# Performance work log

Hardware: AMD Instinct MI355X
Metric: run time of the kernel (lower is better)

The kernel has to match this reference:

```python
import jax, jax.numpy as jnp
import numpy as np

H, DH, RK, RD = 16, 128, 512, 64  # num_heads, head_dim, kv_lora_rank, rope_dim


def apply_rope(x, cos, sin):
    # x: [..., L, ..., rope_dim]; cos/sin: [L, rope_dim//2]
    cos = cos[None, :, None, :]
    sin = sin[None, :, None, :]
    x1, x2 = x[..., 0::2], x[..., 1::2]
    out_real = x1 * cos - x2 * sin
    out_imag = x1 * sin + x2 * cos
    return jnp.stack([out_real, out_imag], axis=-1).reshape(x.shape)


def setup_inputs() -> dict:
    key = jax.random.key(0)
    ks = jax.random.split(key, 7)
    B, L, E, MAXLEN = 2, 2048, 2048, 4096
    x = jax.random.normal(ks[0], (B, L, E), dtype=jnp.float32)
    cos_table = jax.random.uniform(ks[1], (MAXLEN, RD // 2), dtype=jnp.float32)
    sin_table = jax.random.uniform(ks[2], (MAXLEN, RD // 2), dtype=jnp.float32)
    wq = jax.random.normal(ks[3], (E, H * (DH + RD)), dtype=jnp.float32) / np.sqrt(E)
    wkv_down = jax.random.normal(ks[4], (E, RK + RD), dtype=jnp.float32) / np.sqrt(E)
    w_up = jax.random.normal(ks[5], (RK, H * (2 * DH + RD)), dtype=jnp.float32) / np.sqrt(RK)
    w_out = jax.random.normal(ks[6], (H * (DH + RD), E), dtype=jnp.float32) / np.sqrt(H * (DH + RD))
    return {"x": x, "cos_table": cos_table, "sin_table": sin_table,
            "wq": wq, "wkv_down": wkv_down, "w_up": w_up, "w_out": w_out}


def reference(x, cos_table, sin_table, wq, wkv_down, w_up, w_out):
    # Prefill path (use_cache=False): idx = 0, kv comes from current tokens only.
    B, L, E = x.shape
    cos = cos_table[:L]
    sin = sin_table[:L]

    # Queries: per-head content part + rope part
    q_all = (x @ wq).reshape(B, L, H, DH + RD)
    q_head, q_rope = q_all[..., :DH], q_all[..., DH:]
    q_rope = apply_rope(q_rope, cos, sin)
    q = jnp.concatenate([q_head, q_rope], axis=-1)  # [B,L,H,DH+RD]

    # Compressed KV latent + shared rope key
    kv_lat = x @ wkv_down                            # [B,L,RK+RD]
    c_kv = kv_lat[..., :RK]
    k_rope = kv_lat[..., RK:]
    k_rope = apply_rope(k_rope[:, :, None, :], cos, sin)[:, :, 0, :]  # [B,L,RD]

    # Up-project latent to per-head K/V
    up = (c_kv @ w_up).reshape(B, L, H, 2 * DH + RD)
    k_head = up[..., :DH]
    v_head = up[..., DH:2 * DH]
    v_rope = up[..., 2 * DH:]
    k_rope_b = jnp.broadcast_to(k_rope[:, :, None, :], (B, L, H, RD))
    k = jnp.concatenate([k_head, k_rope_b], axis=-1)  # [B,L,H,DH+RD]
    v = jnp.concatenate([v_head, v_rope], axis=-1)    # [B,L,H,DH+RD]

    # Causal attention (query_indices = arange(L), key_indices = arange(L))
    scale = 1.0 / jnp.sqrt(jnp.float32(DH + RD))
    scores = jnp.einsum('blhd,bshd->bhls', q, k) * scale
    idxs = jnp.arange(L)
    bias = jnp.where(idxs[:, None] >= idxs[None, :], 0.0, -1000000000.0)
    attn = jax.nn.softmax(scores + bias[None, None, :, :], axis=-1)
    out = jnp.einsum('bhls,bshd->blhd', attn, v)  # [B,L,H,DH+RD]
    return out.reshape(B, L, -1) @ w_out
```

## Files before the change

### kernel.cpp

```cpp
#include <hip/hip_runtime.h>
#include <stdint.h>

#define H_ 16
#define DH_ 128
#define RK_ 512
#define RD_ 64
#define B_ 2
#define L_ 2048
#define E_ 2048
#define DQ_ 192
#define NQ_ (H_*DQ_)
#define NKV_ 576
#define QKVP_ 3840
#define NUP_ (H_*(2*DH_+RD_))
#define M_ (B_*L_)

typedef unsigned short u16;
typedef __bf16 bf16x8 __attribute__((ext_vector_type(8)));
typedef float floatx4 __attribute__((ext_vector_type(4)));

__device__ __forceinline__ u16 f2bf(float f) {
    union { float f; uint32_t u; } v; v.f = f;
    uint32_t u = v.u;
    u = (u + 0x7fffu + ((u >> 16) & 1u)) >> 16;
    return (u16)u;
}
__device__ __forceinline__ float bf2f(u16 b) {
    union { uint32_t u; float f; } v; v.u = ((uint32_t)b) << 16; return v.f;
}
__device__ __forceinline__ uint32_t cvtpk(float lo, float hi) {
    uint32_t r;
    asm("v_cvt_pk_bf16_f32 %0, %1, %2" : "=v"(r) : "v"(lo), "v"(hi));
    return r;
}

__device__ __forceinline__ void gld_lds16(const void* g, void* l) {
    __builtin_amdgcn_global_load_lds((__attribute__((address_space(1))) void*)(g),
                                     (__attribute__((address_space(3))) void*)(l),
                                     16, 0, 0);
}

__global__ void convert_bf16(const float* __restrict__ in, u16* __restrict__ out, int n4) {
    int i = blockIdx.x * blockDim.x + threadIdx.x;
    if (i >= n4) return;
    float4 v = ((const float4*)in)[i];
    uint2 o;
    o.x = cvtpk(v.x, v.y);
    o.y = cvtpk(v.z, v.w);
    ((uint2*)out)[i] = o;
}

__global__ void transpose_all(const float* __restrict__ wq, const float* __restrict__ wkv,
                              const float* __restrict__ wup, const float* __restrict__ wout,
                              u16* __restrict__ wqkvT, u16* __restrict__ wupT,
                              u16* __restrict__ woutT) {
    __shared__ float tile[32][33];
    int bid = blockIdx.x;
    const float* W; u16* Wt; int K, N, bx, by;
    if (bid < 6144)        { W = wq;   Wt = wqkvT;                      K = 2048; N = 3072; bx = bid % 96;  by = bid / 96; }
    else if (bid < 7680)   { int b = bid - 6144; W = wkv;  Wt = wqkvT + (size_t)3072 * 2048; K = 2048; N = 576;  bx = b % 24;  by = b / 24; }
    else if (bid < 10240)  { int b = bid - 7680; W = wup;  Wt = wupT;   K = 512;  N = 5120; bx = b % 160; by = b / 160; }
    else                   { int b = bid - 10240; W = wout; Wt = woutT; K = 3072; N = 2048; bx = b % 64;  by = b / 64; }
    int n0 = bx * 32, k0 = by * 32;
    int tx = threadIdx.x, ty = threadIdx.y;
    for (int i = 0; i < 4; i++) {
        int k = k0 + ty + i * 8, n = n0 + tx;
        tile[ty + i * 8][tx] = (n < N) ? W[(size_t)k * N + n] : 0.f;
    }
    __syncthreads();
    for (int i = 0; i < 4; i++) {
        int n = n0 + ty + i * 8, k = k0 + tx;
        Wt[(size_t)n * K + k] = f2bf(tile[tx][ty + i * 8]);
    }
}

template<bool BF16OUT>
__global__ __launch_bounds__(512, 4) void gemm256(const u16* __restrict__ A,
                                                  const u16* __restrict__ Bt,
                                                  void* __restrict__ Cv,
                                                  int M, int N, int K, int lda) {
    __shared__ __align__(16) u16 As[3][256 * 32];
    __shared__ __align__(16) u16 Bs[3][128 * 32];
    const int tid = threadIdx.x;
    const int wave = tid >> 6, lane = tid & 63;
    const int quad = lane >> 4, l16 = lane & 15;
    const int wm = (wave >> 1) * 64, wn = (wave & 1) * 64;

    int nwg = gridDim.x * gridDim.y;
    int flat = blockIdx.y * gridDim.x + blockIdx.x;
    int q = nwg >> 3, r = nwg & 7;
    int xcd = flat & 7, pos = flat >> 3;
    int wg = (xcd < r) ? xcd * (q + 1) + pos : r * (q + 1) + (xcd - r) * q + pos;
    const int m0 = (wg & 15) * 256;
    const int n0 = (wg >> 4) * 128;

    const u16* Ab = A + (size_t)m0 * lda;
    const u16* Bb = Bt + (size_t)n0 * K;

    const int qsw = (quad ^ ((l16 >> 1) & 3)) * 8;

    floatx4 zero4 = {0.f, 0.f, 0.f, 0.f};
    floatx4 acc[4][4];
#pragma unroll
    for (int i = 0; i < 4; i++)
#pragma unroll
        for (int j = 0; j < 4; j++) acc[i][j] = zero4;

    auto stage = [&](int t, int b) {
        const u16* Ak = Ab + t * 32;
        const u16* Bk = Bb + t * 32;
#pragma unroll
        for (int it = 0; it < 2; ++it) {
            int c = it * 512 + tid;
            int row = c >> 2, blk = c & 3;
            int bg = blk ^ ((row >> 1) & 3);
            gld_lds16(Ak + (size_t)row * lda + bg * 8, As[b] + row * 32 + blk * 8);
        }
        {
            int row = tid >> 2, blk = tid & 3;
            int bg = blk ^ ((row >> 1) & 3);
            gld_lds16(Bk + (size_t)row * K + bg * 8, Bs[b] + row * 32 + blk * 8);
        }
    };

    const int NT = K >> 5;
    stage(0, 0);
    stage(1, 1);
    int rb = 0;
    for (int t = 0; t < NT; ++t) {
        if (t + 2 < NT) {
            stage(t + 2, rb ? rb - 1 : 2);
            asm volatile("s_waitcnt vmcnt(6)" ::: "memory");
        } else if (t + 1 < NT) {
            asm volatile("s_waitcnt vmcnt(3)" ::: "memory");
        } else {
            asm volatile("s_waitcnt vmcnt(0)" ::: "memory");
        }
        __builtin_amdgcn_s_barrier();

        const u16* Ar = As[rb];
        const u16* Br = Bs[rb];
        bf16x8 af[4], bfv[4];
#pragma unroll
        for (int i = 0; i < 4; i++) af[i]  = *(const bf16x8*)(Ar + (wm + i * 16 + l16) * 32 + qsw);
#pragma unroll
        for (int j = 0; j < 4; j++) bfv[j] = *(const bf16x8*)(Br + (wn + j * 16 + l16) * 32 + qsw);
        __builtin_amdgcn_s_setprio(1);
#pragma unroll
        for (int i = 0; i < 4; i++)
#pragma unroll
            for (int j = 0; j < 4; j++)
                acc[i][j] = __builtin_amdgcn_mfma_f32_16x16x32_bf16(af[i], bfv[j], acc[i][j], 0, 0, 0);
        __builtin_amdgcn_s_setprio(0);
        __builtin_amdgcn_s_barrier();
        rb = (rb == 2) ? 0 : rb + 1;
    }

#pragma unroll
    for (int i = 0; i < 4; i++)
#pragma unroll
        for (int j = 0; j < 4; j++) {
            int mrow = m0 + wm + i * 16 + quad * 4;
            int ncol = n0 + wn + j * 16 + l16;
            if (BF16OUT) {
                u16* Cp = (u16*)Cv + (size_t)mrow * N + ncol;
                for (int rr = 0; rr < 4; rr++) Cp[(size_t)rr * N] = f2bf(acc[i][j][rr]);
            } else {
                float* Cp = (float*)Cv + (size_t)mrow * N + ncol;
                for (int rr = 0; rr < 4; rr++) Cp[(size_t)rr * N] = acc[i][j][rr];
            }
        }
}

__global__ void build_qckv(const u16* __restrict__ qkv, const float* __restrict__ cosT,
                           const float* __restrict__ sinT, u16* __restrict__ qb,
                           u16* __restrict__ kropeb) {
    const float QS = 0.07216878364870323f * 1.4426950408889634f;
    int idx = blockIdx.x * blockDim.x + threadIdx.x;
    const int NQTH = M_ * H_ * 96;
    if (idx < NQTH) {
        int p = idx % 96; int t = idx / 96; int h = t % H_; int row = t / H_;
        int l = row & (L_ - 1); int b = row >> 11;
        const u16* src = qkv + (size_t)row * QKVP_ + h * DQ_;
        u16* dst = qb + ((size_t)(b * H_ + h) * L_ + l) * DQ_;
        int d = 2 * p;
        uint32_t w = *(const uint32_t*)(src + d);
        float x1 = bf2f((u16)(w & 0xffff)), x2 = bf2f((u16)(w >> 16));
        uint32_t o;
        if (d < DH_) o = cvtpk(x1 * QS, x2 * QS);
        else {
            int i = (d - DH_) >> 1;
            float c = cosT[(size_t)l * 32 + i], s = sinT[(size_t)l * 32 + i];
            o = cvtpk((x1 * c - x2 * s) * QS, (x1 * s + x2 * c) * QS);
        }
        *(uint32_t*)(dst + d) = o;
    } else {
        idx -= NQTH;
        if (idx >= M_ * 32) return;
        int i = idx & 31; int row = idx >> 5;
        int l = row & (L_ - 1);
        uint32_t w = *(const uint32_t*)(qkv + (size_t)row * QKVP_ + NQ_ + RK_ + 2 * i);
        float x1 = bf2f((u16)(w & 0xffff)), x2 = bf2f((u16)(w >> 16));
        float c = cosT[(size_t)l * 32 + i], s = sinT[(size_t)l * 32 + i];
        *(uint32_t*)(kropeb + (size_t)row * RD_ + 2 * i) = cvtpk(x1 * c - x2 * s, x1 * s + x2 * c);
    }
}

__global__ __launch_bounds__(256) void build_kvt(const u16* __restrict__ up,
        const u16* __restrict__ kropeb, u16* __restrict__ kb, u16* __restrict__ vtb) {
    __shared__ u16 vt[64][193];
    int blk = blockIdx.x;
    int lt = blk & 31; int bh = blk >> 5; int h = bh % H_; int b = bh / H_;
    int tid = threadIdx.x;
    int l0 = lt * 64;
    for (int it = 0; it < 48; ++it) {
        int idx = it * 256 + tid;
        int lr = idx / 192, d = idx % 192;
        size_t row = (size_t)b * L_ + l0 + lr;
        u16 vv = (d < DH_) ? up[row * NUP_ + h * 320 + DH_ + d]
                           : up[row * NUP_ + h * 320 + 2 * DH_ + (d - DH_)];
        vt[lr][d] = vv;
        u16 kbf = (d < DH_) ? up[row * NUP_ + h * 320 + d]
                            : kropeb[row * RD_ + (d - DH_)];
        kb[((size_t)bh * L_ + l0 + lr) * DQ_ + d] = kbf;
    }
    __syncthreads();
    for (int it = 0; it < 48; ++it) {
        int idx = it * 256 + tid;
        int lr = idx & 63, d = idx >> 6;
        int l = l0 + lr;
        int s5 = l & 31;
        int k5 = ((s5 >> 2) & 3) * 8 + ((s5 >> 4) & 1) * 4 + (s5 & 3);
        int lp = (l & ~31) | k5;
        vtb[((size_t)bh * DQ_ + d) * L_ + lp] = vt[lr][d];
    }
}

__global__ __launch_bounds__(512, 2) void attn(const u16* __restrict__ qb,
        const u16* __restrict__ kb, const u16* __restrict__ vtb,
        u16* __restrict__ po0, u16* __restrict__ po1,
        float* __restrict__ pm0, float* __restrict__ pl0,
        float* __restrict__ pm1, float* __restrict__ pl1) {
    __shared__ __align__(16) u16 Ks[2][64 * 192];
    __shared__ __align__(16) u16 Vs[2][192 * 64];
    int id = blockIdx.x;
    int bh = id & 31, tj = id >> 5;
    int t = tj >> 1, j = tj & 1;
    int tid = threadIdx.x, wave = tid >> 6, lane = tid & 63;
    int quad = lane >> 4, l16 = lane & 15;

    const int x7 = l16 & 7;
    const int h2 = (x7 >> 2) & 1;
    const int qx = quad ^ (x7 & 3);
    const int oA = h2 * 32 + qx * 8;
    const int oB = (1 - h2) * 32 + qx * 8;

    u16* po = j ? po1 : po0;
    float* pm = j ? pm1 : pm0;
    float* pl = j ? pl1 : pl0;

    const u16* kbase0 = kb + (size_t)bh * L_ * DQ_;
    const u16* vbase0 = vtb + (size_t)bh * (size_t)DQ_ * L_;
    floatx4 zero4 = {0.f, 0.f, 0.f, 0.f};

    auto stageKV = [&](int st, int buf) {
        const u16* kg = kbase0 + (size_t)st * 64 * DQ_;
        u16* kd = &Ks[buf][0];
        for (int it = 0; it < 3; ++it) {
            int c = it * 512 + tid;
            int s = c / 24, blk = c - s * 24;
            int blog = (blk & 24) | ((blk & 7) ^ (s & 7));
            gld_lds16(kg + (size_t)s * DQ_ + blog * 8, kd + c * 8);
        }
        const u16* vg = vbase0 + st * 64;
        u16* vd = &Vs[buf][0];
        for (int it = 0; it < 3; ++it) {
            int c = it * 512 + tid;
            int d = c >> 3, blk = c & 7;
            int blog = blk ^ (d & 7);
            gld_lds16(vg + (size_t)d * L_ + blog * 8, vd + c * 8);
        }
    };

    for (int seg = 0; seg < 2; ++seg) {
        const int QT = seg == 0 ? (7 - t) : t;
        const int st0 = j ? (2 * QT + 2) : 0;
        const int st1 = j ? (4 * QT + 3) : (2 * QT + 1);

        bf16x8 aq[2][6];
        const u16* qbase = qb + ((size_t)bh * L_ + QT * 256 + wave * 16 + l16) * DQ_;
        for (int a = 0; a < 2; a++)
            for (int kk = 0; kk < 6; kk++)
                aq[a][kk] = *(const bf16x8*)(qbase + a * 128 * DQ_ + kk * 32 + quad * 8);

        floatx4 o[2][12];
        for (int a = 0; a < 2; a++) for (int i = 0; i < 12; i++) o[a][i] = zero4;
        float m_i[2] = {-INFINITY, -INFINITY};
        float l_i[2] = {0.f, 0.f};

        int cur = 0;
        stageKV(st0, 0);

        for (int st = st0; st <= st1; ++st) {
            if (st < st1) {
                stageKV(st + 1, cur ^ 1);
                asm volatile("s_waitcnt vmcnt(6)" ::: "memory");
            } else {
                asm volatile("s_waitcnt vmcnt(0)" ::: "memory");
            }
            __builtin_amdgcn_s_barrier();
            const u16* Kc = &Ks[cur][0];
            const u16* Vc = &Vs[cur][0];

            int R0 = QT * 256 + wave * 16 - st * 64;
            int R1 = R0 + 128;
            int smax0 = min(3, (R0 + 15) >> 4);
            int smax1 = min(3, (R1 + 15) >> 4);
            bool live0 = smax0 >= 0, live1 = smax1 >= 0;

            float pv[2][4][4];
            float mxa[2] = {-INFINITY, -INFINITY};
#pragma unroll
            for (int stile = 0; stile < 4; ++stile) {
                if (stile > smax1) {
                    for (int r = 0; r < 4; r++) { pv[0][stile][r] = 0.f; pv[1][stile][r] = 0.f; }
                    continue;
                }
                bool do0 = (stile <= smax0);
                floatx4 s1v = zero4, s0v = zero4;
#pragma unroll
                for (int kk = 0; kk < 6; kk++) {
                    int off = (kk >> 1) * 64 + ((kk & 1) ? oB : oA);
                    bf16x8 kf = *(const bf16x8*)(Kc + (stile * 16 + l16) * 192 + off);
                    s1v = __builtin_amdgcn_mfma_f32_16x16x32_bf16(kf, aq[1][kk], s1v, 0, 0, 0);
                    if (do0) s0v = __builtin_amdgcn_mfma_f32_16x16x32_bf16(kf, aq[0][kk], s0v, 0, 0, 0);
                }
                int sb = stile * 16;
                if (sb + 15 > R1) {
                    for (int r = 0; r < 4; r++) {
                        float v = (sb + quad * 4 + r > R1 + l16) ? -1e30f : s1v[r];
                        pv[1][stile][r] = v; mxa[1] = fmaxf(mxa[1], v);
                    }
                } else {
                    for (int r = 0; r < 4; r++) { pv[1][stile][r] = s1v[r]; mxa[1] = fmaxf(mxa[1], s1v[r]); }
                }
                if (do0) {
                    if (sb + 15 > R0) {
                        for (int r = 0; r < 4; r++) {
                            float v = (sb + quad * 4 + r > R0 + l16) ? -1e30f : s0v[r];
                            pv[0][stile][r] = v; mxa[0] = fmaxf(mxa[0], v);
                        }
                    } else {
                        for (int r = 0; r < 4; r++) { pv[0][stile][r] = s0v[r]; mxa[0] = fmaxf(mxa[0], s0v[r]); }
                    }
                } else {
                    for (int r = 0; r < 4; r++) pv[0][stile][r] = 0.f;
                }
            }

            bf16x8 pf[2][2];
            bool lv[2] = {live0, live1};
            int smx[2] = {smax0, smax1};
#pragma unroll
            for (int a = 0; a < 2; a++) {
                if (!lv[a]) continue;
                float mx = mxa[a];
                mx = fmaxf(mx, __shfl_xor(mx, 16));
                mx = fmaxf(mx, __shfl_xor(mx, 32));
                float mn;
                if (__all(mx <= m_i[a] + 8.0f)) {
                    mn = m_i[a];
                } else {
                    mn = fmaxf(m_i[a], mx);
                    float alpha = exp2f(m_i[a] - mn);
                    m_i[a] = mn;
                    l_i[a] *= alpha;
                    for (int i = 0; i < 12; i++) o[a][i] *= alpha;
                }
                float rs = 0.f;
#pragma unroll
                for (int stile = 0; stile < 4; ++stile) {
                    if (stile > smx[a]) continue;
                    for (int r = 0; r < 4; r++) {
                        float e = exp2f(pv[a][stile][r] - mn);
                        pv[a][stile][r] = e;
                        rs += e;
                    }
                }
                rs += __shfl_xor(rs, 16);
                rs += __shfl_xor(rs, 32);
                l_i[a] += rs;
                for (int g = 0; g < 2; g++) {
                    union { bf16x8 v; u16 s[8]; } u;
                    for (int r = 0; r < 4; r++) {
                        u.s[r]     = f2bf(pv[a][g * 2][r]);
                        u.s[4 + r] = f2bf(pv[a][g * 2 + 1][r]);
                    }
                    pf[a][g] = u.v;
                }
            }

            for (int g = 0; g < 2; g++) {
                int vo = g ? oB : oA;
#pragma unroll
                for (int dtile = 0; dtile < 12; dtile++) {
                    bf16x8 vf = *(const bf16x8*)(Vc + (dtile * 16 + l16) * 64 + vo);
                    if (live0)
                        o[0][dtile] = __builtin_amdgcn_mfma_f32_16x16x32_bf16(vf, pf[0][g], o[0][dtile], 0, 0, 0);
                    if (live1)
                        o[1][dtile] = __builtin_amdgcn_mfma_f32_16x16x32_bf16(vf, pf[1][g], o[1][dtile], 0, 0, 0);
                }
            }
            __builtin_amdgcn_s_barrier();
            cur ^= 1;
        }

        int tile = bh * 8 + QT;
        for (int a = 0; a < 2; a++) {
            int q = a * 128 + wave * 16 + l16;
            u16* dst = po + ((size_t)tile * 256 + q) * 192;
            for (int dtile = 0; dtile < 12; dtile++) {
                ushort4 pk;
                pk.x = f2bf(o[a][dtile][0]);
                pk.y = f2bf(o[a][dtile][1]);
                pk.z = f2bf(o[a][dtile][2]);
                pk.w = f2bf(o[a][dtile][3]);
                *(ushort4*)(dst + dtile * 16 + quad * 4) = pk;
            }
            if (quad == 0) {
                pm[(size_t)tile * 256 + q] = m_i[a];
                pl[(size_t)tile * 256 + q] = l_i[a];
            }
        }
        __syncthreads();
    }
}

__global__ void attn_merge(const u16* __restrict__ po0, const u16* __restrict__ po1,
                           const float* __restrict__ pm0, const float* __restrict__ pl0,
                           const float* __restrict__ pm1, const float* __restrict__ pl1,
                           u16* __restrict__ ao) {
    int idx = blockIdx.x * blockDim.x + threadIdx.x;
    int c = idx % 48; int rest = idx / 48;
    int q = rest & 255; int tile = rest >> 8;
    int bh = tile >> 3, QT = tile & 7;
    size_t mi = (size_t)tile * 256 + q;
    float m0 = pm0[mi], m1 = pm1[mi];
    float l0 = pl0[mi], l1 = pl1[mi];
    float m = fmaxf(m0, m1);
    float a0 = exp2f(m0 - m), a1 = exp2f(m1 - m);
    float inv = 1.0f / (l0 * a0 + l1 * a1);
    float s0 = a0 * inv, s1 = a1 * inv;
    ushort4 u0 = *(const ushort4*)(po0 + mi * 192 + c * 4);
    ushort4 u1 = *(const ushort4*)(po1 + mi * 192 + c * 4);
    int b = bh >> 4, h = bh & 15;
    int l = QT * 256 + q;
    u16* dst = ao + (((size_t)(b * L_ + l)) * H_ + h) * DQ_ + c * 4;
    uint2 pk2;
    pk2.x = cvtpk(bf2f(u0.x) * s0 + bf2f(u1.x) * s1, bf2f(u0.y) * s0 + bf2f(u1.y) * s1);
    pk2.y = cvtpk(bf2f(u0.z) * s0 + bf2f(u1.z) * s1, bf2f(u0.w) * s0 + bf2f(u1.w) * s1);
    *(uint2*)dst = pk2;
}

extern "C" void kernel_launch(void* const* d_in, const int* in_sizes, int n_in,
                              void* d_out, int out_size, void* d_ws, size_t ws_size,
                              hipStream_t stream) {
    const float* x    = (const float*)d_in[0];
    const float* cosT = (const float*)d_in[1];
    const float* sinT = (const float*)d_in[2];
    const float* wq   = (const float*)d_in[3];
    const float* wkv  = (const float*)d_in[4];
    const float* wup  = (const float*)d_in[5];
    const float* wout = (const float*)d_in[6];
    float* out = (float*)d_out;
    char* ws = (char*)d_ws;

    size_t off = 0;
    auto alloc = [&](size_t b) { size_t r = off; off += (b + 255) & ~(size_t)255; return r; };
    u16* xb     = (u16*)(ws + alloc((size_t)M_ * E_ * 2));
    u16* wqkvT  = (u16*)(ws + alloc((size_t)QKVP_ * E_ * 2));
    u16* wupT   = (u16*)(ws + alloc((size_t)NUP_ * RK_ * 2));
    u16* woutT  = (u16*)(ws + alloc((size_t)E_ * NQ_ * 2));
    u16* qb     = (u16*)(ws + alloc((size_t)B_ * H_ * L_ * DQ_ * 2));
    u16* kb     = (u16*)(ws + alloc((size_t)B_ * H_ * L_ * DQ_ * 2));
    u16* vtb    = (u16*)(ws + alloc((size_t)B_ * H_ * DQ_ * L_ * 2));
    u16* ao     = (u16*)(ws + alloc((size_t)M_ * NQ_ * 2));
    u16* kropeb = (u16*)(ws + alloc((size_t)M_ * RD_ * 2));
    char* scratch = ws + alloc((size_t)M_ * NUP_ * 4);
    u16* qkvb = (u16*)(scratch);
    size_t qkvSz = ((size_t)M_ * QKVP_ * 2 + 255) & ~(size_t)255;
    u16* upb  = (u16*)(scratch + qkvSz);
    size_t poSz = (size_t)256 * 256 * 192 * 2;
    u16*   po0 = (u16*)(scratch);
    u16*   po1 = (u16*)(scratch + poSz);
    float* pm0 = (float*)(scratch + 2 * poSz);
    float* pl0 = (float*)(scratch + 2 * poSz + 256 * 256 * 4);
    float* pm1 = (float*)(scratch + 2 * poSz + 2 * 256 * 256 * 4);
    float* pl1 = (float*)(scratch + 2 * poSz + 3 * 256 * 256 * 4);

    dim3 tb(32, 8);
    int n4 = M_ * E_ / 4;
    convert_bf16<<<(n4 + 255) / 256, 256, 0, stream>>>(x, xb, n4);
    transpose_all<<<16384, tb, 0, stream>>>(wq, wkv, wup, wout, wqkvT, wupT, woutT);

    gemm256<true><<<dim3(QKVP_ / 128, M_ / 256), 512, 0, stream>>>(xb, wqkvT, qkvb, M_, QKVP_, E_, E_);

    int nb = (M_ * H_ * 96 + M_ * 32 + 255) / 256;
    build_qckv<<<nb, 256, 0, stream>>>(qkvb, cosT, sinT, qb, kropeb);

    gemm256<true><<<dim3(NUP_ / 128, M_ / 256), 512, 0, stream>>>(qkvb + NQ_, wupT, upb, M_, NUP_, RK_, QKVP_);
    build_kvt<<<B_ * H_ * 32, 256, 0, stream>>>(upb, kropeb, kb, vtb);

    attn<<<256, 512, 0, stream>>>(qb, kb, vtb, po0, po1, pm0, pl0, pm1, pl1);
    attn_merge<<<(256 * 256 * 48) / 256, 256, 0, stream>>>(po0, po1, pm0, pl0, pm1, pl1, ao);

    gemm256<false><<<dim3(E_ / 128, M_ / 256), 512, 0, stream>>>(ao, woutT, out, M_, E_, NQ_, NQ_);
}
```

Baseline: 494.4 us.

## Split attention KV range four ways and single-buffer V in LDS

The attention kernel now splits each query tile's causal key range into four partitions instead of two and doubles the grid, producing four partial outputs that the merge kernel combines with log-sum-exp rescaling. V staging becomes single-buffered and is issued after the K prefetch, with waits placed just before the PV MFMAs, which cuts shared memory per block. Launch bounds are raised to four blocks per CU. The aim is more parallel blocks across the CUs. The risks are a tighter register budget that may force spills, more partial-output traffic through the merge, and exposed V load latency. One partial buffer reuses the workspace region of the bf16 input and transposed weights, which are no longer needed at that stage.

Measured after the change: 968.5 us. +95.9%, slower.

```diff
diff --git a/kernel.cpp b/kernel.cpp
--- a/kernel.cpp
+++ b/kernel.cpp
@@ -236,16 +236,15 @@
     }
 }
 
-__global__ __launch_bounds__(512, 2) void attn(const u16* __restrict__ qb,
+__global__ __launch_bounds__(512, 4) void attn(const u16* __restrict__ qb,
         const u16* __restrict__ kb, const u16* __restrict__ vtb,
-        u16* __restrict__ po0, u16* __restrict__ po1,
-        float* __restrict__ pm0, float* __restrict__ pl0,
-        float* __restrict__ pm1, float* __restrict__ pl1) {
+        u16* __restrict__ poA, u16* __restrict__ poS,
+        float* __restrict__ pmB, float* __restrict__ plB) {
     __shared__ __align__(16) u16 Ks[2][64 * 192];
-    __shared__ __align__(16) u16 Vs[2][192 * 64];
+    __shared__ __align__(16) u16 Vs[192 * 64];
     int id = blockIdx.x;
     int bh = id & 31, tj = id >> 5;
-    int t = tj >> 1, j = tj & 1;
+    int t = tj >> 2, j = tj & 3;
     int tid = threadIdx.x, wave = tid >> 6, lane = tid & 63;
     int quad = lane >> 4, l16 = lane & 15;
 
@@ -255,15 +254,16 @@
     const int oA = h2 * 32 + qx * 8;
     const int oB = (1 - h2) * 32 + qx * 8;
 
-    u16* po = j ? po1 : po0;
-    float* pm = j ? pm1 : pm0;
-    float* pl = j ? pl1 : pl0;
+    const size_t poSzE = (size_t)256 * 256 * 192;
+    u16* po = (j == 0) ? poA : poS + (size_t)(j - 1) * poSzE;
+    float* pm = pmB + (size_t)j * 65536;
+    float* pl = plB + (size_t)j * 65536;
 
     const u16* kbase0 = kb + (size_t)bh * L_ * DQ_;
     const u16* vbase0 = vtb + (size_t)bh * (size_t)DQ_ * L_;
     floatx4 zero4 = {0.f, 0.f, 0.f, 0.f};
 
-    auto stageKV = [&](int st, int buf) {
+    auto stageK = [&](int st, int buf) {
         const u16* kg = kbase0 + (size_t)st * 64 * DQ_;
         u16* kd = &Ks[buf][0];
         for (int it = 0; it < 3; ++it) {
@@ -272,20 +272,21 @@
             int blog = (blk & 24) | ((blk & 7) ^ (s & 7));
             gld_lds16(kg + (size_t)s * DQ_ + blog * 8, kd + c * 8);
         }
+    };
+    auto stageV = [&](int st) {
         const u16* vg = vbase0 + st * 64;
-        u16* vd = &Vs[buf][0];
         for (int it = 0; it < 3; ++it) {
             int c = it * 512 + tid;
             int d = c >> 3, blk = c & 7;
             int blog = blk ^ (d & 7);
-            gld_lds16(vg + (size_t)d * L_ + blog * 8, vd + c * 8);
+            gld_lds16(vg + (size_t)d * L_ + blog * 8, Vs + c * 8);
         }
     };
 
     for (int seg = 0; seg < 2; ++seg) {
         const int QT = seg == 0 ? (7 - t) : t;
-        const int st0 = j ? (2 * QT + 2) : 0;
-        const int st1 = j ? (4 * QT + 3) : (2 * QT + 1);
+        const int st0 = j * (QT + 1);
+        const int st1 = st0 + QT;
 
         bf16x8 aq[2][6];
         const u16* qbase = qb + ((size_t)bh * L_ + QT * 256 + wave * 16 + l16) * DQ_;
@@ -299,18 +300,14 @@
         float l_i[2] = {0.f, 0.f};
 
         int cur = 0;
-        stageKV(st0, 0);
+        stageK(st0, 0);
+        asm volatile("s_waitcnt vmcnt(0)" ::: "memory");
+        __builtin_amdgcn_s_barrier();
 
         for (int st = st0; st <= st1; ++st) {
-            if (st < st1) {
-                stageKV(st + 1, cur ^ 1);
-                asm volatile("s_waitcnt vmcnt(6)" ::: "memory");
-            } else {
-                asm volatile("s_waitcnt vmcnt(0)" ::: "memory");
-            }
-            __builtin_amdgcn_s_barrier();
+            stageV(st);
+            if (st < st1) stageK(st + 1, cur ^ 1);
             const u16* Kc = &Ks[cur][0];
-            const u16* Vc = &Vs[cur][0];
 
             int R0 = QT * 256 + wave * 16 - st * 64;
             int R1 = R0 + 128;
@@ -400,17 +397,22 @@
                 }
             }
 
+            if (st < st1) { asm volatile("s_waitcnt vmcnt(3)" ::: "memory"); }
+            else          { asm volatile("s_waitcnt vmcnt(0)" ::: "memory"); }
+            __builtin_amdgcn_s_barrier();
+
             for (int g = 0; g < 2; g++) {
                 int vo = g ? oB : oA;
 #pragma unroll
                 for (int dtile = 0; dtile < 12; dtile++) {
-                    bf16x8 vf = *(const bf16x8*)(Vc + (dtile * 16 + l16) * 64 + vo);
+                    bf16x8 vf = *(const bf16x8*)(Vs + (dtile * 16 + l16) * 64 + vo);
                     if (live0)
                         o[0][dtile] = __builtin_amdgcn_mfma_f32_16x16x32_bf16(vf, pf[0][g], o[0][dtile], 0, 0, 0);
                     if (live1)
                         o[1][dtile] = __builtin_amdgcn_mfma_f32_16x16x32_bf16(vf, pf[1][g], o[1][dtile], 0, 0, 0);
                 }
             }
+            asm volatile("s_waitcnt vmcnt(0)" ::: "memory");
             __builtin_amdgcn_s_barrier();
             cur ^= 1;
         }
@@ -436,29 +438,39 @@
     }
 }
 
-__global__ void attn_merge(const u16* __restrict__ po0, const u16* __restrict__ po1,
-                           const float* __restrict__ pm0, const float* __restrict__ pl0,
-                           const float* __restrict__ pm1, const float* __restrict__ pl1,
+__global__ void attn_merge(const u16* __restrict__ poA, const u16* __restrict__ poS,
+                           const float* __restrict__ pmB, const float* __restrict__ plB,
                            u16* __restrict__ ao) {
     int idx = blockIdx.x * blockDim.x + threadIdx.x;
     int c = idx % 48; int rest = idx / 48;
     int q = rest & 255; int tile = rest >> 8;
     int bh = tile >> 3, QT = tile & 7;
     size_t mi = (size_t)tile * 256 + q;
-    float m0 = pm0[mi], m1 = pm1[mi];
-    float l0 = pl0[mi], l1 = pl1[mi];
-    float m = fmaxf(m0, m1);
-    float a0 = exp2f(m0 - m), a1 = exp2f(m1 - m);
-    float inv = 1.0f / (l0 * a0 + l1 * a1);
-    float s0 = a0 * inv, s1 = a1 * inv;
-    ushort4 u0 = *(const ushort4*)(po0 + mi * 192 + c * 4);
-    ushort4 u1 = *(const ushort4*)(po1 + mi * 192 + c * 4);
+    const size_t poSzE = (size_t)256 * 256 * 192;
+    float mj[4], lj[4];
+    float m = -INFINITY;
+    for (int jj = 0; jj < 4; jj++) {
+        mj[jj] = pmB[(size_t)jj * 65536 + mi];
+        lj[jj] = plB[(size_t)jj * 65536 + mi];
+        m = fmaxf(m, mj[jj]);
+    }
+    float aj[4], denom = 0.f;
+    for (int jj = 0; jj < 4; jj++) { aj[jj] = exp2f(mj[jj] - m); denom += lj[jj] * aj[jj]; }
+    float inv = 1.0f / denom;
+    float acc0 = 0.f, acc1 = 0.f, acc2 = 0.f, acc3 = 0.f;
+    for (int jj = 0; jj < 4; jj++) {
+        const u16* pj = (jj == 0) ? poA : poS + (size_t)(jj - 1) * poSzE;
+        ushort4 u0 = *(const ushort4*)(pj + mi * 192 + c * 4);
+        float s = aj[jj] * inv;
+        acc0 += bf2f(u0.x) * s; acc1 += bf2f(u0.y) * s;
+        acc2 += bf2f(u0.z) * s; acc3 += bf2f(u0.w) * s;
+    }
     int b = bh >> 4, h = bh & 15;
     int l = QT * 256 + q;
     u16* dst = ao + (((size_t)(b * L_ + l)) * H_ + h) * DQ_ + c * 4;
     uint2 pk2;
-    pk2.x = cvtpk(bf2f(u0.x) * s0 + bf2f(u1.x) * s1, bf2f(u0.y) * s0 + bf2f(u1.y) * s1);
-    pk2.y = cvtpk(bf2f(u0.z) * s0 + bf2f(u1.z) * s1, bf2f(u0.w) * s0 + bf2f(u1.w) * s1);
+    pk2.x = cvtpk(acc0, acc1);
+    pk2.y = cvtpk(acc2, acc3);
     *(uint2*)dst = pk2;
 }
 
@@ -491,12 +503,10 @@
     size_t qkvSz = ((size_t)M_ * QKVP_ * 2 + 255) & ~(size_t)255;
     u16* upb  = (u16*)(scratch + qkvSz);
     size_t poSz = (size_t)256 * 256 * 192 * 2;
-    u16*   po0 = (u16*)(scratch);
-    u16*   po1 = (u16*)(scratch + poSz);
-    float* pm0 = (float*)(scratch + 2 * poSz);
-    float* pl0 = (float*)(scratch + 2 * poSz + 256 * 256 * 4);
-    float* pm1 = (float*)(scratch + 2 * poSz + 2 * 256 * 256 * 4);
-    float* pl1 = (float*)(scratch + 2 * poSz + 3 * 256 * 256 * 4);
+    u16*   poA = (u16*)(ws);
+    u16*   poS = (u16*)(scratch);
+    float* pmB = (float*)(scratch + 3 * poSz);
+    float* plB = (float*)(scratch + 3 * poSz + 4 * 65536 * 4);
 
     dim3 tb(32, 8);
     int n4 = M_ * E_ / 4;
@@ -511,8 +521,8 @@
     gemm256<true><<<dim3(NUP_ / 128, M_ / 256), 512, 0, stream>>>(qkvb + NQ_, wupT, upb, M_, NUP_, RK_, QKVP_);
     build_kvt<<<B_ * H_ * 32, 256, 0, stream>>>(upb, kropeb, kb, vtb);
 
-    attn<<<256, 512, 0, stream>>>(qb, kb, vtb, po0, po1, pm0, pl0, pm1, pl1);
-    attn_merge<<<(256 * 256 * 48) / 256, 256, 0, stream>>>(po0, po1, pm0, pl0, pm1, pl1, ao);
+    attn<<<512, 512, 0, stream>>>(qb, kb, vtb, poA, poS, pmB, plB);
+    attn_merge<<<(256 * 256 * 48) / 256, 256, 0, stream>>>(poA, poS, pmB, plB, ao);
 
     gemm256<false><<<dim3(E_ / 128, M_ / 256), 512, 0, stream>>>(ao, woutT, out, M_, E_, NQ_, NQ_);
 }
```
